# Kernel tuning notes

Measured on AMD Instinct MI355X. Metric: run time of the kernel, lower is better.

## Reference

```python
import jax, jax.numpy as jnp
import numpy as np

N = 50000
E = 800000
IN, H, OUT = 128, 96, 64
BN_EPS = 1e-5


def setup_inputs() -> dict:
    key = jax.random.key(0)
    ks = jax.random.split(key, 16)
    x = jax.random.normal(ks[0], (N, IN), dtype=jnp.float32)
    edge_index = jax.random.randint(ks[1], (2, E), 0, N, dtype=jnp.int64)
    edge_weight = jax.random.uniform(ks[2], (E,), dtype=jnp.float32)
    def lin(k, fo, fi):
        # PyG glorot-ish init
        s = 1.0 / np.sqrt(fi)
        return jax.random.uniform(k, (fo, fi), minval=-s, maxval=s, dtype=jnp.float32)
    W1, b1 = lin(ks[3], H, IN), jnp.zeros((H,), jnp.float32)
    W2, b2 = lin(ks[4], H, H), jnp.zeros((H,), jnp.float32)
    W3, b3 = lin(ks[5], OUT, H), jnp.zeros((OUT,), jnp.float32)
    g1 = jnp.ones((H,), jnp.float32); beta1 = jnp.zeros((H,), jnp.float32)
    m1 = 0.1 * jax.random.normal(ks[6], (H,), dtype=jnp.float32)
    v1 = jnp.abs(1.0 + 0.1 * jax.random.normal(ks[7], (H,), dtype=jnp.float32))
    g2 = jnp.ones((H,), jnp.float32); beta2 = jnp.zeros((H,), jnp.float32)
    m2 = 0.1 * jax.random.normal(ks[8], (H,), dtype=jnp.float32)
    v2 = jnp.abs(1.0 + 0.1 * jax.random.normal(ks[9], (H,), dtype=jnp.float32))
    return dict(x=x, edge_index=edge_index, edge_weight=edge_weight,
                W1=W1, b1=b1, W2=W2, b2=b2, W3=W3, b3=b3,
                g1=g1, beta1=beta1, m1=m1, v1=v1,
                g2=g2, beta2=beta2, m2=m2, v2=v2)


def gcn_norm(edge_index, edge_weight, n):
    # PyG gcn_norm with add_self_loops=True, fill_value=1.0
    loop = jnp.arange(n, dtype=edge_index.dtype)
    row = jnp.concatenate([edge_index[0], loop])  # sources
    col = jnp.concatenate([edge_index[1], loop])  # targets
    ew = jnp.concatenate([edge_weight, jnp.ones((n,), edge_weight.dtype)])
    deg = jax.ops.segment_sum(ew, col, num_segments=n)
    dis = jnp.where(deg > 0, jax.lax.rsqrt(deg), 0.0)  # inf -> 0 masked_fill
    norm = dis[row] * ew * dis[col]
    return row, col, norm


def gcn_conv(x, row, col, norm, W, b, n):
    xw = x @ W.T                       # [N, F_out] dense transform first
    msg = norm[:, None] * xw[row]      # [E+N, F_out] gather + edge scale
    out = jax.ops.segment_sum(msg, col, num_segments=n)  # scatter-add
    return out + b


def bn_eval(x, gamma, beta, mean, var):
    return (x - mean) * jax.lax.rsqrt(var + BN_EPS) * gamma + beta


def reference(x, edge_index, edge_weight, W1, b1, W2, b2, W3, b3,
              g1, beta1, m1, v1, g2, beta2, m2, v2):
    n = x.shape[0]
    row, col, norm = gcn_norm(edge_index, edge_weight, n)  # cached=True: shared
    h = gcn_conv(x, row, col, norm, W1, b1, n)
    h = jax.nn.relu(bn_eval(h, g1, beta1, m1, v1))
    h = gcn_conv(h, row, col, norm, W2, b2, n)
    h = jax.nn.relu(bn_eval(h, g2, beta2, m2, v2))
    out = gcn_conv(h, row, col, norm, W3, b3, n)
    return out
```

## Files before the change

kernel.cpp:

```cpp
#include <hip/hip_runtime.h>
#include <hip/hip_fp16.h>


constexpr float BN_EPS = 1e-5f;
constexpr float DEG_SCALE = 131072.0f;
constexpr float INV_DEG_SCALE = 1.0f / 131072.0f;
constexpr float NORM_SCALE = 32768.0f;
constexpr float INV_NORM_SCALE = 1.0f / 32768.0f;

typedef _Float16 f16x8 __attribute__((ext_vector_type(8)));
typedef float f32x4 __attribute__((ext_vector_type(4)));


__device__ __forceinline__ void gemm1_q(const float* __restrict__ x,
                                        const float* __restrict__ W1,
                                        unsigned char* __restrict__ t1q,
                                        float* __restrict__ scl1,
                                        int n0b, int tid, int n,
                                        _Float16* lds, unsigned* rmaxb) {
    constexpr int LROW = 104;
    constexpr int WROW = 136;
    if (tid < 64) rmaxb[tid] = 0u;
    for (int i = tid; i < 96 * 128; i += 256) {
        int row = i >> 7, col = i & 127;
        lds[row * WROW + col] = (_Float16)W1[i];
    }
    __syncthreads();

    int wave = tid >> 6, lane = tid & 63, quad = lane >> 4, r = lane & 15;
    int n0 = n0b + wave * 16;
    bool active = (n0 < n);
    f32x4 acc[6];
    if (active) {
        f16x8 a[4];
        const float* xr = x + (size_t)(n0 + r) * 128 + quad * 8;
#pragma unroll
        for (int kt = 0; kt < 4; ++kt) {
            float4 v0 = *(const float4*)(xr + kt * 32);
            float4 v1 = *(const float4*)(xr + kt * 32 + 4);
            f16x8 t = {(_Float16)v0.x, (_Float16)v0.y, (_Float16)v0.z, (_Float16)v0.w,
                       (_Float16)v1.x, (_Float16)v1.y, (_Float16)v1.z, (_Float16)v1.w};
            a[kt] = t;
        }
#pragma unroll
        for (int ft = 0; ft < 6; ++ft) acc[ft] = (f32x4){0.f, 0.f, 0.f, 0.f};
#pragma unroll
        for (int kt = 0; kt < 4; ++kt) {
#pragma unroll
            for (int ft = 0; ft < 6; ++ft) {
                f16x8 b = *(const f16x8*)(lds + (size_t)(ft * 16 + r) * WROW + kt * 32 + quad * 8);
                acc[ft] = __builtin_amdgcn_mfma_f32_16x16x32_f16(a[kt], b, acc[ft], 0, 0, 0);
            }
        }
    }
    __syncthreads();
    if (active) {
#pragma unroll
        for (int ft = 0; ft < 6; ++ft)
#pragma unroll
            for (int reg = 0; reg < 4; ++reg)
                lds[(size_t)(wave * 16 + quad * 4 + reg) * LROW + ft * 16 + r] =
                    (_Float16)acc[ft][reg];
    }
    __syncthreads();
    {
        int row = tid >> 2, qt = tid & 3;
        const _Float16* lp = lds + (size_t)row * LROW + qt * 24;
        float mx = 0.f;
#pragma unroll
        for (int j = 0; j < 24; ++j) mx = fmaxf(mx, fabsf((float)lp[j]));
        atomicMax(&rmaxb[row], __float_as_uint(mx));
    }
    __syncthreads();
    for (int i = tid; i < 64 * 12; i += 256) {
        int row = i / 12, c = i - row * 12;
        int grow = n0b + row;
        if (grow >= n) continue;
        float rm = __uint_as_float(rmaxb[row]);
        float inv = (rm > 0.f) ? 127.0f / rm : 0.f;
        const _Float16* lp = lds + (size_t)row * LROW + c * 8;
        unsigned lo = 0, hi = 0;
#pragma unroll
        for (int j = 0; j < 4; ++j) {
            int qv = __float2int_rn((float)lp[j] * inv);
            qv = qv > 127 ? 127 : (qv < -127 ? -127 : qv);
            lo |= ((unsigned)qv & 255u) << (8 * j);
        }
#pragma unroll
        for (int j = 0; j < 4; ++j) {
            int qv = __float2int_rn((float)lp[4 + j] * inv);
            qv = qv > 127 ? 127 : (qv < -127 ? -127 : qv);
            hi |= ((unsigned)qv & 255u) << (8 * j);
        }
        *(uint2*)(t1q + (size_t)grow * 96 + c * 8) = make_uint2(lo, hi);
        if (c == 0) scl1[grow] = rm * (1.0f / 127.0f);
    }
}


__global__ __launch_bounds__(256) void k_mega(
    const int* __restrict__ row_idx, const int* __restrict__ col_idx,
    const float* __restrict__ ew,
    unsigned long long* packed, unsigned char* rank, int e_cnt, int pair_b,
    int t1, int t2,
    const float* __restrict__ x, const float* __restrict__ W1,
    unsigned char* __restrict__ t1q, float* __restrict__ scl1, int n,
    const float* __restrict__ W2, const float* __restrict__ W3,
    _Float16* __restrict__ w2h, _Float16* __restrict__ w3h,
    int w2n4, int w3n4) {
    __shared__ _Float16 lds[96 * 136];
    __shared__ unsigned rmaxb[64];
    int b = blockIdx.x;
    if (b < 2 * pair_b) {
        int q = b >> 1;
        if ((b & 1) == 0) {
#pragma unroll
            for (int j = 0; j < 4; ++j) {
                int e = q * 1024 + j * 256 + (int)threadIdx.x;
                if (e < e_cnt) {
                    int c = col_idx[e];
                    int r = row_idx[e];
                    int t = (r >= t2) ? 2 : ((r >= t1) ? 1 : 0);
                    int sh = 24 + 10 * t;
                    unsigned wfix = (unsigned)(ew[e] * DEG_SCALE + 0.5f);
                    unsigned long long inc = (1ull << sh) | (unsigned long long)wfix;
                    unsigned long long old = atomicAdd(&packed[c], inc);
                    rank[e] = (unsigned char)((old >> sh) & 0x3FFull);
                }
            }
        } else {
            gemm1_q(x, W1, t1q, scl1, q * 64, (int)threadIdx.x, n, lds, rmaxb);
        }
    } else {
        int i = (b - 2 * pair_b) * 256 + (int)threadIdx.x;
        const float* src; _Float16* dst; int o;
        if (i < w2n4) { src = W2; dst = w2h; o = i; }
        else if (i < w2n4 + w3n4) { src = W3; dst = w3h; o = i - w2n4; }
        else return;
        float4 v = ((const float4*)src)[o];
        __half2 h0 = __floats2half2_rn(v.x, v.y);
        __half2 h1 = __floats2half2_rn(v.z, v.w);
        *(uint2*)(dst + (size_t)o * 4) = make_uint2(*(unsigned*)&h0, *(unsigned*)&h1);
    }
}


__device__ __forceinline__ int pk_cnt(unsigned long long p) {
    return (int)((p >> 24) & 0x3FF) + (int)((p >> 34) & 0x3FF) + (int)((p >> 44) & 0x3FF);
}

__global__ void k_scan1(const unsigned long long* __restrict__ packed,
                        int* bsum, float* dis, int n) {
    __shared__ int s[256];
    int i = blockIdx.x * 256 + threadIdx.x;
    int cnt = 0;
    if (i < n) {
        unsigned long long p = packed[i];
        cnt = pk_cnt(p);
        float wsum = (float)(unsigned)(p & 0xFFFFFFull) * INV_DEG_SCALE;
        dis[i] = rsqrtf(1.0f + wsum);
    }
    s[threadIdx.x] = cnt;
    __syncthreads();
    for (int off = 128; off > 0; off >>= 1) {
        if ((int)threadIdx.x < off) s[threadIdx.x] += s[threadIdx.x + off];
        __syncthreads();
    }
    if (threadIdx.x == 0) bsum[blockIdx.x] = s[0];
}

__global__ void k_scan23(const unsigned long long* __restrict__ packed,
                         const int* __restrict__ bsum,
                         int* row_ptr, int n, int e_total, int nb) {
    __shared__ int sb[256];
    __shared__ int s[256];
    int t = threadIdx.x;
    int bv = (t < nb) ? bsum[t] : 0;
    sb[t] = bv;
    __syncthreads();
    for (int off = 1; off < 256; off <<= 1) {
        int x = (t >= off) ? sb[t - off] : 0;
        __syncthreads();
        sb[t] += x;
        __syncthreads();
    }
    int boff = (blockIdx.x == 0) ? 0 : sb[blockIdx.x - 1];

    int i = blockIdx.x * 256 + t;
    int v = (i < n) ? pk_cnt(packed[i]) : 0;
    s[t] = v;
    __syncthreads();
    for (int off = 1; off < 256; off <<= 1) {
        int x = (t >= off) ? s[t - off] : 0;
        __syncthreads();
        s[t] += x;
        __syncthreads();
    }
    int ex = s[t] - v + boff;
    if (i < n) row_ptr[i] = ex;
    if (i == 0) row_ptr[n] = e_total;
}

__global__ void k_fill(const int* __restrict__ row_idx, const int* __restrict__ col_idx,
                       const float* __restrict__ ew, const float* __restrict__ dis,
                       const int* __restrict__ row_ptr, const unsigned char* __restrict__ rank,
                       const unsigned long long* __restrict__ packed,
                       unsigned* ep, int e_cnt, int t1, int t2) {
    int e = blockIdx.x * 256 + threadIdx.x;
    if (e < e_cnt) {
        int r = row_idx[e];
        int c = col_idx[e];
        unsigned long long p = packed[c];
        int c0 = (int)((p >> 24) & 0x3FF);
        int c1 = (int)((p >> 34) & 0x3FF);
        int t = (r >= t2) ? 2 : ((r >= t1) ? 1 : 0);
        int off = (t > 0 ? c0 : 0) + (t > 1 ? c1 : 0);
        float nm = dis[r] * ew[e];
        unsigned q = (unsigned)(nm * NORM_SCALE + 0.5f);
        if (q > 65535u) q = 65535u;
        ep[row_ptr[c] + off + (int)rank[e]] = ((unsigned)r << 16) | q;
    }
}


__device__ inline void cvt8(uint4 u, float* f) {
    float2 t;
    t = __half22float2(*(const __half2*)&u.x); f[0] = t.x; f[1] = t.y;
    t = __half22float2(*(const __half2*)&u.y); f[2] = t.x; f[3] = t.y;
    t = __half22float2(*(const __half2*)&u.z); f[4] = t.x; f[5] = t.y;
    t = __half22float2(*(const __half2*)&u.w); f[6] = t.x; f[7] = t.y;
}

__device__ inline void h8_acc(uint4 u, float w, float acc[8]) {
    float2 a = __half22float2(*(const __half2*)&u.x);
    float2 b = __half22float2(*(const __half2*)&u.y);
    float2 c = __half22float2(*(const __half2*)&u.z);
    float2 d = __half22float2(*(const __half2*)&u.w);
    acc[0] = fmaf(w, a.x, acc[0]); acc[1] = fmaf(w, a.y, acc[1]);
    acc[2] = fmaf(w, b.x, acc[2]); acc[3] = fmaf(w, b.y, acc[3]);
    acc[4] = fmaf(w, c.x, acc[4]); acc[5] = fmaf(w, c.y, acc[5]);
    acc[6] = fmaf(w, d.x, acc[6]); acc[7] = fmaf(w, d.y, acc[7]);
}

__device__ inline void q8_acc(uint2 v, float ws, float acc[8]) {
    int a = (int)v.x, b = (int)v.y;
    acc[0] = fmaf(ws, (float)(int)(char)(a      ), acc[0]);
    acc[1] = fmaf(ws, (float)(int)(char)(a >>  8), acc[1]);
    acc[2] = fmaf(ws, (float)(int)(char)(a >> 16), acc[2]);
    acc[3] = fmaf(ws, (float)(a >> 24),            acc[3]);
    acc[4] = fmaf(ws, (float)(int)(char)(b      ), acc[4]);
    acc[5] = fmaf(ws, (float)(int)(char)(b >>  8), acc[5]);
    acc[6] = fmaf(ws, (float)(int)(char)(b >> 16), acc[6]);
    acc[7] = fmaf(ws, (float)(b >> 24),            acc[7]);
}

__device__ __forceinline__ void gather_row_q(const unsigned char* __restrict__ tq,
                                             const float* __restrict__ scl,
                                             const unsigned* __restrict__ ep,
                                             int e0, int e1, int q, float acc[8]) {
    int e = e0;
    for (; e + 4 <= e1; e += 4) {
        unsigned p0 = ep[e + 0], p1 = ep[e + 1], p2 = ep[e + 2], p3 = ep[e + 3];
        uint2 v0 = *(const uint2*)(tq + (size_t)(p0 >> 16) * 96 + q * 8);
        uint2 v1 = *(const uint2*)(tq + (size_t)(p1 >> 16) * 96 + q * 8);
        uint2 v2 = *(const uint2*)(tq + (size_t)(p2 >> 16) * 96 + q * 8);
        uint2 v3 = *(const uint2*)(tq + (size_t)(p3 >> 16) * 96 + q * 8);
        float s0 = scl[p0 >> 16], s1 = scl[p1 >> 16];
        float s2 = scl[p2 >> 16], s3 = scl[p3 >> 16];
        q8_acc(v0, (float)(p0 & 0xffffu) * INV_NORM_SCALE * s0, acc);
        q8_acc(v1, (float)(p1 & 0xffffu) * INV_NORM_SCALE * s1, acc);
        q8_acc(v2, (float)(p2 & 0xffffu) * INV_NORM_SCALE * s2, acc);
        q8_acc(v3, (float)(p3 & 0xffffu) * INV_NORM_SCALE * s3, acc);
    }
    for (; e < e1; ++e) {
        unsigned p = ep[e];
        uint2 v = *(const uint2*)(tq + (size_t)(p >> 16) * 96 + q * 8);
        q8_acc(v, (float)(p & 0xffffu) * INV_NORM_SCALE * scl[p >> 16], acc);
    }
}

template <int FQ>
__device__ __forceinline__ void gather_row(const uint4* __restrict__ base,
                                           const unsigned* __restrict__ ep,
                                           int e0, int e1, int q, float acc[8]) {
    int e = e0;
    for (; e + 8 <= e1; e += 8) {
        unsigned p0 = ep[e + 0], p1 = ep[e + 1], p2 = ep[e + 2], p3 = ep[e + 3];
        unsigned p4 = ep[e + 4], p5 = ep[e + 5], p6 = ep[e + 6], p7 = ep[e + 7];
        uint4 x0 = base[(size_t)(p0 >> 16) * FQ + q];
        uint4 x1 = base[(size_t)(p1 >> 16) * FQ + q];
        uint4 x2 = base[(size_t)(p2 >> 16) * FQ + q];
        uint4 x3 = base[(size_t)(p3 >> 16) * FQ + q];
        uint4 x4 = base[(size_t)(p4 >> 16) * FQ + q];
        uint4 x5 = base[(size_t)(p5 >> 16) * FQ + q];
        uint4 x6 = base[(size_t)(p6 >> 16) * FQ + q];
        uint4 x7 = base[(size_t)(p7 >> 16) * FQ + q];
        h8_acc(x0, (float)(p0 & 0xffffu) * INV_NORM_SCALE, acc);
        h8_acc(x1, (float)(p1 & 0xffffu) * INV_NORM_SCALE, acc);
        h8_acc(x2, (float)(p2 & 0xffffu) * INV_NORM_SCALE, acc);
        h8_acc(x3, (float)(p3 & 0xffffu) * INV_NORM_SCALE, acc);
        h8_acc(x4, (float)(p4 & 0xffffu) * INV_NORM_SCALE, acc);
        h8_acc(x5, (float)(p5 & 0xffffu) * INV_NORM_SCALE, acc);
        h8_acc(x6, (float)(p6 & 0xffffu) * INV_NORM_SCALE, acc);
        h8_acc(x7, (float)(p7 & 0xffffu) * INV_NORM_SCALE, acc);
    }
    for (; e + 4 <= e1; e += 4) {
        unsigned p0 = ep[e + 0], p1 = ep[e + 1], p2 = ep[e + 2], p3 = ep[e + 3];
        uint4 x0 = base[(size_t)(p0 >> 16) * FQ + q];
        uint4 x1 = base[(size_t)(p1 >> 16) * FQ + q];
        uint4 x2 = base[(size_t)(p2 >> 16) * FQ + q];
        uint4 x3 = base[(size_t)(p3 >> 16) * FQ + q];
        h8_acc(x0, (float)(p0 & 0xffffu) * INV_NORM_SCALE, acc);
        h8_acc(x1, (float)(p1 & 0xffffu) * INV_NORM_SCALE, acc);
        h8_acc(x2, (float)(p2 & 0xffffu) * INV_NORM_SCALE, acc);
        h8_acc(x3, (float)(p3 & 0xffffu) * INV_NORM_SCALE, acc);
    }
    for (; e < e1; ++e) {
        unsigned p = ep[e];
        uint4 xv = base[(size_t)(p >> 16) * FQ + q];
        h8_acc(xv, (float)(p & 0xffffu) * INV_NORM_SCALE, acc);
    }
}


template <int FOUT, bool QOUT>
__global__ __launch_bounds__(192) void k_aggr_mm(
    const unsigned char* __restrict__ tq, const float* __restrict__ scl,
    const int* __restrict__ row_ptr, const unsigned* __restrict__ ep,
    const float* __restrict__ dis, const float* __restrict__ bias,
    const float* __restrict__ g, const float* __restrict__ beta,
    const float* __restrict__ m, const float* __restrict__ v,
    const _Float16* __restrict__ Wh,
    void* __restrict__ Yout, float* __restrict__ sclo, int n) {
    constexpr int LROW = 104;
    __shared__ _Float16 lds[16 * LROW];
    __shared__ unsigned rmaxb[16];
    int tid = (int)threadIdx.x;
    int n0b = blockIdx.x * 16;
    int nl = tid / 12;
    int q = tid - nl * 12;
    int node = n0b + nl;
    if (QOUT && tid < 16) rmaxb[tid] = 0u;

    if (node < n) {
        float d = dis[node];
        float acc[8];
#pragma unroll
        for (int j = 0; j < 8; ++j) acc[j] = 0.f;
        {
            uint2 sv = *(const uint2*)(tq + (size_t)node * 96 + q * 8);
            q8_acc(sv, d * scl[node], acc);
        }
        gather_row_q(tq, scl, ep, row_ptr[node], row_ptr[node + 1], q, acc);

        int fb = q * 8;
        const float4* bb = (const float4*)(bias + fb);
        float4 b0 = bb[0], b1 = bb[1];
        acc[0] = fmaf(acc[0], d, b0.x); acc[1] = fmaf(acc[1], d, b0.y);
        acc[2] = fmaf(acc[2], d, b0.z); acc[3] = fmaf(acc[3], d, b0.w);
        acc[4] = fmaf(acc[4], d, b1.x); acc[5] = fmaf(acc[5], d, b1.y);
        acc[6] = fmaf(acc[6], d, b1.z); acc[7] = fmaf(acc[7], d, b1.w);
#pragma unroll
        for (int j = 0; j < 8; ++j) {
            acc[j] = fmaxf((acc[j] - m[fb + j]) * rsqrtf(v[fb + j] + BN_EPS) * g[fb + j]
                           + beta[fb + j], 0.f);
        }
        __half2 h0 = __floats2half2_rn(acc[0], acc[1]);
        __half2 h1 = __floats2half2_rn(acc[2], acc[3]);
        __half2 h2 = __floats2half2_rn(acc[4], acc[5]);
        __half2 h3 = __floats2half2_rn(acc[6], acc[7]);
        *(uint4*)(lds + (size_t)nl * LROW + fb) =
            make_uint4(*(unsigned*)&h0, *(unsigned*)&h1, *(unsigned*)&h2, *(unsigned*)&h3);
    }
    __syncthreads();

    constexpr int FT = FOUT / 16;
    f32x4 cacc[FT];
    int quad = tid >> 4, r = tid & 15;
    if (tid < 64) {
        f16x8 a[3];
#pragma unroll
        for (int kt = 0; kt < 3; ++kt)
            a[kt] = *(const f16x8*)(lds + (size_t)r * LROW + kt * 32 + quad * 8);
#pragma unroll
        for (int ft = 0; ft < FT; ++ft) cacc[ft] = (f32x4){0.f, 0.f, 0.f, 0.f};
#pragma unroll
        for (int kt = 0; kt < 3; ++kt) {
#pragma unroll
            for (int ft = 0; ft < FT; ++ft) {
                f16x8 b = *(const f16x8*)(Wh + (size_t)(ft * 16 + r) * 96 + kt * 32 + quad * 8);
                cacc[ft] = __builtin_amdgcn_mfma_f32_16x16x32_f16(a[kt], b, cacc[ft], 0, 0, 0);
            }
        }
    }
    __syncthreads();
    if (tid < 64) {
#pragma unroll
        for (int ft = 0; ft < FT; ++ft)
#pragma unroll
            for (int reg = 0; reg < 4; ++reg)
                lds[(size_t)(quad * 4 + reg) * LROW + ft * 16 + r] = (_Float16)cacc[ft][reg];
    }
    __syncthreads();

    if (QOUT) {
        if (tid < 64) {
            int row = tid >> 2, qt = tid & 3;
            const _Float16* lp = lds + (size_t)row * LROW + qt * 24;
            float mx = 0.f;
#pragma unroll
            for (int j = 0; j < 24; ++j) mx = fmaxf(mx, fabsf((float)lp[j]));
            atomicMax(&rmaxb[row], __float_as_uint(mx));
        }
        __syncthreads();
        {
            int row = nl, c = q;
            int grow = n0b + row;
            if (grow < n) {
                float rm = __uint_as_float(rmaxb[row]);
                float inv = (rm > 0.f) ? 127.0f / rm : 0.f;
                const _Float16* lp = lds + (size_t)row * LROW + c * 8;
                unsigned lo = 0, hi = 0;
#pragma unroll
                for (int j = 0; j < 4; ++j) {
                    int qv = __float2int_rn((float)lp[j] * inv);
                    qv = qv > 127 ? 127 : (qv < -127 ? -127 : qv);
                    lo |= ((unsigned)qv & 255u) << (8 * j);
                }
#pragma unroll
                for (int j = 0; j < 4; ++j) {
                    int qv = __float2int_rn((float)lp[4 + j] * inv);
                    qv = qv > 127 ? 127 : (qv < -127 ? -127 : qv);
                    hi |= ((unsigned)qv & 255u) << (8 * j);
                }
                *(uint2*)((unsigned char*)Yout + (size_t)grow * 96 + c * 8) =
                    make_uint2(lo, hi);
                if (c == 0) sclo[grow] = rm * (1.0f / 127.0f);
            }
        }
    } else {
        constexpr int CPR = FOUT / 8;
        for (int i = tid; i < 16 * CPR; i += 192) {
            int row = i / CPR, c = i - row * CPR;
            int grow = n0b + row;
            if (grow < n)
                *(uint4*)((_Float16*)Yout + (size_t)grow * FOUT + c * 8) =
                    *(const uint4*)(lds + (size_t)row * LROW + c * 8);
        }
    }
}


__global__ __launch_bounds__(256) void k_aggr3(
    const _Float16* __restrict__ xw, const int* __restrict__ row_ptr,
    const unsigned* __restrict__ ep,
    const float* __restrict__ dis, const float* __restrict__ bias,
    float* __restrict__ out, int n) {
    constexpr int FQ = 8;
    int tg = blockIdx.x * 256 + threadIdx.x;
    int node = tg / FQ;
    int q = tg - node * FQ;
    if (node >= n) return;

    const uint4* __restrict__ base = (const uint4*)xw;
    float d = dis[node];
    float acc[8];
    {
        uint4 sv = base[(size_t)node * FQ + q];
        float t[8];
        cvt8(sv, t);
#pragma unroll
        for (int j = 0; j < 8; ++j) acc[j] = d * t[j];
    }
    gather_row<FQ>(base, ep, row_ptr[node], row_ptr[node + 1], q, acc);

    int fb = q * 8;
    const float4* bb = (const float4*)(bias + fb);
    float4 b0 = bb[0], b1 = bb[1];
    acc[0] = fmaf(acc[0], d, b0.x); acc[1] = fmaf(acc[1], d, b0.y);
    acc[2] = fmaf(acc[2], d, b0.z); acc[3] = fmaf(acc[3], d, b0.w);
    acc[4] = fmaf(acc[4], d, b1.x); acc[5] = fmaf(acc[5], d, b1.y);
    acc[6] = fmaf(acc[6], d, b1.z); acc[7] = fmaf(acc[7], d, b1.w);

    float* op = out + (size_t)node * 64 + fb;
    *(float4*)(op + 0) = make_float4(acc[0], acc[1], acc[2], acc[3]);
    *(float4*)(op + 4) = make_float4(acc[4], acc[5], acc[6], acc[7]);
}


extern "C" void kernel_launch(void* const* d_in, const int* in_sizes, int n_in,
                              void* d_out, int out_size, void* d_ws, size_t ws_size,
                              hipStream_t stream) {
    constexpr int IN = 128, H = 96, OUT = 64;

    const float* x   = (const float*)d_in[0];
    const int*   ei  = (const int*)d_in[1];
    const float* ew  = (const float*)d_in[2];
    const float* W1  = (const float*)d_in[3];
    const float* b1  = (const float*)d_in[4];
    const float* W2  = (const float*)d_in[5];
    const float* b2  = (const float*)d_in[6];
    const float* W3  = (const float*)d_in[7];
    const float* b3  = (const float*)d_in[8];
    const float* g1  = (const float*)d_in[9];
    const float* be1 = (const float*)d_in[10];
    const float* m1  = (const float*)d_in[11];
    const float* v1  = (const float*)d_in[12];
    const float* g2  = (const float*)d_in[13];
    const float* be2 = (const float*)d_in[14];
    const float* m2  = (const float*)d_in[15];
    const float* v2  = (const float*)d_in[16];

    const int N = in_sizes[0] / IN;
    const int E = in_sizes[2];
    const int* row_idx = ei;
    const int* col_idx = ei + E;
    const int T1 = N / 3, T2 = 2 * (N / 3);

    char* ws = (char*)d_ws;
    size_t off = 0;
    auto alloc = [&](size_t bytes) -> void* {
        void* p = ws + off;
        off = (off + bytes + 255) & ~(size_t)255;
        return p;
    };
    unsigned long long* packed = (unsigned long long*)alloc((size_t)N * 8);
    float*     dis     = (float*)alloc((size_t)N * 4);
    int*       row_ptr = (int*)alloc((size_t)(N + 1) * 4);
    int*       bsum    = (int*)alloc(256 * 4);
    unsigned char* rank = (unsigned char*)alloc((size_t)E);
    unsigned*  ep      = (unsigned*)alloc((size_t)E * 4);
    _Float16*  w2h     = (_Float16*)alloc((size_t)H * H * 2);
    _Float16*  w3h     = (_Float16*)alloc((size_t)OUT * H * 2);
    unsigned char* t1q = (unsigned char*)alloc((size_t)N * 96);
    float*     scl1    = (float*)alloc((size_t)N * 4);
    unsigned char* t2q = (unsigned char*)alloc((size_t)N * 96);
    float*     scl2    = (float*)alloc((size_t)N * 4);
    _Float16*  buf64   = (_Float16*)alloc((size_t)N * OUT * 2);
    (void)ws_size; (void)n_in; (void)out_size;

    constexpr int W2N4 = H * H / 4, W3N4 = OUT * H / 4;
    const int NB = (N + 255) / 256;
    const int DEG1024 = (E + 1023) / 1024;
    const int GG = (N + 63) / 64;
    const int PAIR = (DEG1024 > GG) ? DEG1024 : GG;
    const int CVT_B = (W2N4 + W3N4 + 255) / 256;

    hipMemsetAsync(packed, 0, (size_t)N * 8, stream);
    k_mega<<<2 * PAIR + CVT_B, 256, 0, stream>>>(
        row_idx, col_idx, ew, packed, rank, E, PAIR, T1, T2,
        x, W1, t1q, scl1, N, W2, W3, w2h, w3h, W2N4, W3N4);
    k_scan1<<<NB, 256, 0, stream>>>(packed, bsum, dis, N);
    k_scan23<<<NB, 256, 0, stream>>>(packed, bsum, row_ptr, N, E, NB);
    k_fill<<<(E + 255) / 256, 256, 0, stream>>>(row_idx, col_idx, ew, dis,
                                                row_ptr, rank, packed, ep, E, T1, T2);

    const int GF = (N + 15) / 16;
    const int GA64 = ((size_t)N * (OUT / 8) + 255) / 256;

    k_aggr_mm<H, true><<<GF, 192, 0, stream>>>(
        t1q, scl1, row_ptr, ep, dis, b1, g1, be1, m1, v1, w2h, t2q, scl2, N);

    k_aggr_mm<OUT, false><<<GF, 192, 0, stream>>>(
        t2q, scl2, row_ptr, ep, dis, b2, g2, be2, m2, v2, w3h, buf64, nullptr, N);

    k_aggr3<<<GA64, 256, 0, stream>>>(buf64, row_ptr, ep, dis, b3, (float*)d_out, N);
}
```

Measured before the change: 238.7 us.

## Widen int8 gather to 16 features per thread and process 32 nodes per block

The fused aggregate+matmul kernels now have each thread gather 16 int8 features with one 16-byte load instead of 8 with an 8-byte load, so six threads cover a 96-wide row. Each 192-thread block now handles 32 nodes, two waves run the MFMA transform, and the quantize/store phase is rewritten as a strided loop. This halves the number of edge-index and scale loads per node feature and doubles work per block. The cost is more registers per thread and half as many blocks and threads in flight for the latency-bound gathers.

New measurement: 246.9 us. 1.03x slower.

```diff
diff --git a/kernel.cpp b/kernel.cpp
--- a/kernel.cpp
+++ b/kernel.cpp
@@ -242,40 +242,48 @@
     acc[6] = fmaf(w, d.x, acc[6]); acc[7] = fmaf(w, d.y, acc[7]);
 }
 
-__device__ inline void q8_acc(uint2 v, float ws, float acc[8]) {
-    int a = (int)v.x, b = (int)v.y;
-    acc[0] = fmaf(ws, (float)(int)(char)(a      ), acc[0]);
-    acc[1] = fmaf(ws, (float)(int)(char)(a >>  8), acc[1]);
-    acc[2] = fmaf(ws, (float)(int)(char)(a >> 16), acc[2]);
-    acc[3] = fmaf(ws, (float)(a >> 24),            acc[3]);
-    acc[4] = fmaf(ws, (float)(int)(char)(b      ), acc[4]);
-    acc[5] = fmaf(ws, (float)(int)(char)(b >>  8), acc[5]);
-    acc[6] = fmaf(ws, (float)(int)(char)(b >> 16), acc[6]);
-    acc[7] = fmaf(ws, (float)(b >> 24),            acc[7]);
-}
-
-__device__ __forceinline__ void gather_row_q(const unsigned char* __restrict__ tq,
-                                             const float* __restrict__ scl,
-                                             const unsigned* __restrict__ ep,
-                                             int e0, int e1, int q, float acc[8]) {
+__device__ inline void q16_acc(uint4 v, float ws, float acc[16]) {
+    int a = (int)v.x, b = (int)v.y, c = (int)v.z, d = (int)v.w;
+    acc[0]  = fmaf(ws, (float)(int)(char)(a      ), acc[0]);
+    acc[1]  = fmaf(ws, (float)(int)(char)(a >>  8), acc[1]);
+    acc[2]  = fmaf(ws, (float)(int)(char)(a >> 16), acc[2]);
+    acc[3]  = fmaf(ws, (float)(a >> 24),            acc[3]);
+    acc[4]  = fmaf(ws, (float)(int)(char)(b      ), acc[4]);
+    acc[5]  = fmaf(ws, (float)(int)(char)(b >>  8), acc[5]);
+    acc[6]  = fmaf(ws, (float)(int)(char)(b >> 16), acc[6]);
+    acc[7]  = fmaf(ws, (float)(b >> 24),            acc[7]);
+    acc[8]  = fmaf(ws, (float)(int)(char)(c      ), acc[8]);
+    acc[9]  = fmaf(ws, (float)(int)(char)(c >>  8), acc[9]);
+    acc[10] = fmaf(ws, (float)(int)(char)(c >> 16), acc[10]);
+    acc[11] = fmaf(ws, (float)(c >> 24),            acc[11]);
+    acc[12] = fmaf(ws, (float)(int)(char)(d      ), acc[12]);
+    acc[13] = fmaf(ws, (float)(int)(char)(d >>  8), acc[13]);
+    acc[14] = fmaf(ws, (float)(int)(char)(d >> 16), acc[14]);
+    acc[15] = fmaf(ws, (float)(d >> 24),            acc[15]);
+}
+
+__device__ __forceinline__ void gather_row_q16(const unsigned char* __restrict__ tq,
+                                               const float* __restrict__ scl,
+                                               const unsigned* __restrict__ ep,
+                                               int e0, int e1, int q, float acc[16]) {
     int e = e0;
     for (; e + 4 <= e1; e += 4) {
         unsigned p0 = ep[e + 0], p1 = ep[e + 1], p2 = ep[e + 2], p3 = ep[e + 3];
-        uint2 v0 = *(const uint2*)(tq + (size_t)(p0 >> 16) * 96 + q * 8);
-        uint2 v1 = *(const uint2*)(tq + (size_t)(p1 >> 16) * 96 + q * 8);
-        uint2 v2 = *(const uint2*)(tq + (size_t)(p2 >> 16) * 96 + q * 8);
-        uint2 v3 = *(const uint2*)(tq + (size_t)(p3 >> 16) * 96 + q * 8);
+        uint4 v0 = *(const uint4*)(tq + (size_t)(p0 >> 16) * 96 + q * 16);
+        uint4 v1 = *(const uint4*)(tq + (size_t)(p1 >> 16) * 96 + q * 16);
+        uint4 v2 = *(const uint4*)(tq + (size_t)(p2 >> 16) * 96 + q * 16);
+        uint4 v3 = *(const uint4*)(tq + (size_t)(p3 >> 16) * 96 + q * 16);
         float s0 = scl[p0 >> 16], s1 = scl[p1 >> 16];
         float s2 = scl[p2 >> 16], s3 = scl[p3 >> 16];
-        q8_acc(v0, (float)(p0 & 0xffffu) * INV_NORM_SCALE * s0, acc);
-        q8_acc(v1, (float)(p1 & 0xffffu) * INV_NORM_SCALE * s1, acc);
-        q8_acc(v2, (float)(p2 & 0xffffu) * INV_NORM_SCALE * s2, acc);
-        q8_acc(v3, (float)(p3 & 0xffffu) * INV_NORM_SCALE * s3, acc);
+        q16_acc(v0, (float)(p0 & 0xffffu) * INV_NORM_SCALE * s0, acc);
+        q16_acc(v1, (float)(p1 & 0xffffu) * INV_NORM_SCALE * s1, acc);
+        q16_acc(v2, (float)(p2 & 0xffffu) * INV_NORM_SCALE * s2, acc);
+        q16_acc(v3, (float)(p3 & 0xffffu) * INV_NORM_SCALE * s3, acc);
     }
     for (; e < e1; ++e) {
         unsigned p = ep[e];
-        uint2 v = *(const uint2*)(tq + (size_t)(p >> 16) * 96 + q * 8);
-        q8_acc(v, (float)(p & 0xffffu) * INV_NORM_SCALE * scl[p >> 16], acc);
+        uint4 v = *(const uint4*)(tq + (size_t)(p >> 16) * 96 + q * 16);
+        q16_acc(v, (float)(p & 0xffffu) * INV_NORM_SCALE * scl[p >> 16], acc);
     }
 }
 
@@ -333,55 +341,67 @@
     const _Float16* __restrict__ Wh,
     void* __restrict__ Yout, float* __restrict__ sclo, int n) {
     constexpr int LROW = 104;
-    __shared__ _Float16 lds[16 * LROW];
-    __shared__ unsigned rmaxb[16];
+    __shared__ _Float16 lds[32 * LROW];
+    __shared__ unsigned rmaxb[32];
     int tid = (int)threadIdx.x;
-    int n0b = blockIdx.x * 16;
-    int nl = tid / 12;
-    int q = tid - nl * 12;
+    int n0b = blockIdx.x * 32;
+    int nl = tid / 6;
+    int q = tid - nl * 6;
     int node = n0b + nl;
-    if (QOUT && tid < 16) rmaxb[tid] = 0u;
+    if (QOUT && tid < 32) rmaxb[tid] = 0u;
 
     if (node < n) {
         float d = dis[node];
-        float acc[8];
-#pragma unroll
-        for (int j = 0; j < 8; ++j) acc[j] = 0.f;
+        float acc[16];
+#pragma unroll
+        for (int j = 0; j < 16; ++j) acc[j] = 0.f;
         {
-            uint2 sv = *(const uint2*)(tq + (size_t)node * 96 + q * 8);
-            q8_acc(sv, d * scl[node], acc);
-        }
-        gather_row_q(tq, scl, ep, row_ptr[node], row_ptr[node + 1], q, acc);
-
-        int fb = q * 8;
+            uint4 sv = *(const uint4*)(tq + (size_t)node * 96 + q * 16);
+            q16_acc(sv, d * scl[node], acc);
+        }
+        gather_row_q16(tq, scl, ep, row_ptr[node], row_ptr[node + 1], q, acc);
+
+        int fb = q * 16;
         const float4* bb = (const float4*)(bias + fb);
-        float4 b0 = bb[0], b1 = bb[1];
-        acc[0] = fmaf(acc[0], d, b0.x); acc[1] = fmaf(acc[1], d, b0.y);
-        acc[2] = fmaf(acc[2], d, b0.z); acc[3] = fmaf(acc[3], d, b0.w);
-        acc[4] = fmaf(acc[4], d, b1.x); acc[5] = fmaf(acc[5], d, b1.y);
-        acc[6] = fmaf(acc[6], d, b1.z); acc[7] = fmaf(acc[7], d, b1.w);
-#pragma unroll
-        for (int j = 0; j < 8; ++j) {
+        float4 b0 = bb[0], b1 = bb[1], b2 = bb[2], b3 = bb[3];
+        acc[0]  = fmaf(acc[0],  d, b0.x); acc[1]  = fmaf(acc[1],  d, b0.y);
+        acc[2]  = fmaf(acc[2],  d, b0.z); acc[3]  = fmaf(acc[3],  d, b0.w);
+        acc[4]  = fmaf(acc[4],  d, b1.x); acc[5]  = fmaf(acc[5],  d, b1.y);
+        acc[6]  = fmaf(acc[6],  d, b1.z); acc[7]  = fmaf(acc[7],  d, b1.w);
+        acc[8]  = fmaf(acc[8],  d, b2.x); acc[9]  = fmaf(acc[9],  d, b2.y);
+        acc[10] = fmaf(acc[10], d, b2.z); acc[11] = fmaf(acc[11], d, b2.w);
+        acc[12] = fmaf(acc[12], d, b3.x); acc[13] = fmaf(acc[13], d, b3.y);
+        acc[14] = fmaf(acc[14], d, b3.z); acc[15] = fmaf(acc[15], d, b3.w);
+#pragma unroll
+        for (int j = 0; j < 16; ++j) {
             acc[j] = fmaxf((acc[j] - m[fb + j]) * rsqrtf(v[fb + j] + BN_EPS) * g[fb + j]
                            + beta[fb + j], 0.f);
         }
-        __half2 h0 = __floats2half2_rn(acc[0], acc[1]);
-        __half2 h1 = __floats2half2_rn(acc[2], acc[3]);
-        __half2 h2 = __floats2half2_rn(acc[4], acc[5]);
-        __half2 h3 = __floats2half2_rn(acc[6], acc[7]);
-        *(uint4*)(lds + (size_t)nl * LROW + fb) =
-            make_uint4(*(unsigned*)&h0, *(unsigned*)&h1, *(unsigned*)&h2, *(unsigned*)&h3);
+        _Float16* dst = lds + (size_t)nl * LROW + fb;
+        __half2 h0 = __floats2half2_rn(acc[0],  acc[1]);
+        __half2 h1 = __floats2half2_rn(acc[2],  acc[3]);
+        __half2 h2 = __floats2half2_rn(acc[4],  acc[5]);
+        __half2 h3 = __floats2half2_rn(acc[6],  acc[7]);
+        __half2 h4 = __floats2half2_rn(acc[8],  acc[9]);
+        __half2 h5 = __floats2half2_rn(acc[10], acc[11]);
+        __half2 h6 = __floats2half2_rn(acc[12], acc[13]);
+        __half2 h7 = __floats2half2_rn(acc[14], acc[15]);
+        *(uint4*)(dst + 0) = make_uint4(*(unsigned*)&h0, *(unsigned*)&h1,
+                                        *(unsigned*)&h2, *(unsigned*)&h3);
+        *(uint4*)(dst + 8) = make_uint4(*(unsigned*)&h4, *(unsigned*)&h5,
+                                        *(unsigned*)&h6, *(unsigned*)&h7);
     }
     __syncthreads();
 
     constexpr int FT = FOUT / 16;
     f32x4 cacc[FT];
-    int quad = tid >> 4, r = tid & 15;
-    if (tid < 64) {
+    int w = tid >> 6;
+    int lane = tid & 63, quad = lane >> 4, r = lane & 15;
+    if (w < 2) {
         f16x8 a[3];
 #pragma unroll
         for (int kt = 0; kt < 3; ++kt)
-            a[kt] = *(const f16x8*)(lds + (size_t)r * LROW + kt * 32 + quad * 8);
+            a[kt] = *(const f16x8*)(lds + (size_t)(w * 16 + r) * LROW + kt * 32 + quad * 8);
 #pragma unroll
         for (int ft = 0; ft < FT; ++ft) cacc[ft] = (f32x4){0.f, 0.f, 0.f, 0.f};
 #pragma unroll
@@ -394,17 +414,18 @@
         }
     }
     __syncthreads();
-    if (tid < 64) {
+    if (w < 2) {
 #pragma unroll
         for (int ft = 0; ft < FT; ++ft)
 #pragma unroll
             for (int reg = 0; reg < 4; ++reg)
-                lds[(size_t)(quad * 4 + reg) * LROW + ft * 16 + r] = (_Float16)cacc[ft][reg];
+                lds[(size_t)(w * 16 + quad * 4 + reg) * LROW + ft * 16 + r] =
+                    (_Float16)cacc[ft][reg];
     }
     __syncthreads();
 
     if (QOUT) {
-        if (tid < 64) {
+        if (tid < 128) {
             int row = tid >> 2, qt = tid & 3;
             const _Float16* lp = lds + (size_t)row * LROW + qt * 24;
             float mx = 0.f;
@@ -413,34 +434,33 @@
             atomicMax(&rmaxb[row], __float_as_uint(mx));
         }
         __syncthreads();
-        {
-            int row = nl, c = q;
+        for (int i = tid; i < 32 * 12; i += 192) {
+            int row = i / 12, c = i - row * 12;
             int grow = n0b + row;
-            if (grow < n) {
-                float rm = __uint_as_float(rmaxb[row]);
-                float inv = (rm > 0.f) ? 127.0f / rm : 0.f;
-                const _Float16* lp = lds + (size_t)row * LROW + c * 8;
-                unsigned lo = 0, hi = 0;
-#pragma unroll
-                for (int j = 0; j < 4; ++j) {
-                    int qv = __float2int_rn((float)lp[j] * inv);
-                    qv = qv > 127 ? 127 : (qv < -127 ? -127 : qv);
-                    lo |= ((unsigned)qv & 255u) << (8 * j);
-                }
-#pragma unroll
-                for (int j = 0; j < 4; ++j) {
-                    int qv = __float2int_rn((float)lp[4 + j] * inv);
-                    qv = qv > 127 ? 127 : (qv < -127 ? -127 : qv);
-                    hi |= ((unsigned)qv & 255u) << (8 * j);
-                }
-                *(uint2*)((unsigned char*)Yout + (size_t)grow * 96 + c * 8) =
-                    make_uint2(lo, hi);
-                if (c == 0) sclo[grow] = rm * (1.0f / 127.0f);
+            if (grow >= n) continue;
+            float rm = __uint_as_float(rmaxb[row]);
+            float inv = (rm > 0.f) ? 127.0f / rm : 0.f;
+            const _Float16* lp = lds + (size_t)row * LROW + c * 8;
+            unsigned lo = 0, hi = 0;
+#pragma unroll
+            for (int j = 0; j < 4; ++j) {
+                int qv = __float2int_rn((float)lp[j] * inv);
+                qv = qv > 127 ? 127 : (qv < -127 ? -127 : qv);
+                lo |= ((unsigned)qv & 255u) << (8 * j);
             }
+#pragma unroll
+            for (int j = 0; j < 4; ++j) {
+                int qv = __float2int_rn((float)lp[4 + j] * inv);
+                qv = qv > 127 ? 127 : (qv < -127 ? -127 : qv);
+                hi |= ((unsigned)qv & 255u) << (8 * j);
+            }
+            *(uint2*)((unsigned char*)Yout + (size_t)grow * 96 + c * 8) =
+                make_uint2(lo, hi);
+            if (c == 0) sclo[grow] = rm * (1.0f / 127.0f);
         }
     } else {
         constexpr int CPR = FOUT / 8;
-        for (int i = tid; i < 16 * CPR; i += 192) {
+        for (int i = tid; i < 32 * CPR; i += 192) {
             int row = i / CPR, c = i - row * CPR;
             int grow = n0b + row;
             if (grow < n)
@@ -555,13 +575,13 @@
     k_fill<<<(E + 255) / 256, 256, 0, stream>>>(row_idx, col_idx, ew, dis,
                                                 row_ptr, rank, packed, ep, E, T1, T2);
 
-    const int GF = (N + 15) / 16;
+    const int GF32 = (N + 31) / 32;
     const int GA64 = ((size_t)N * (OUT / 8) + 255) / 256;
 
-    k_aggr_mm<H, true><<<GF, 192, 0, stream>>>(
+    k_aggr_mm<H, true><<<GF32, 192, 0, stream>>>(
         t1q, scl1, row_ptr, ep, dis, b1, g1, be1, m1, v1, w2h, t2q, scl2, N);
 
-    k_aggr_mm<OUT, false><<<GF, 192, 0, stream>>>(
+    k_aggr_mm<OUT, false><<<GF32, 192, 0, stream>>>(
         t2q, scl2, row_ptr, ep, dis, b2, g2, be2, m2, v2, w3h, buf64, nullptr, N);
 
     k_aggr3<<<GA64, 256, 0, stream>>>(buf64, row_ptr, ep, dis, b3, (float*)d_out, N);
```
